# Kernel tuning notes

Hardware: AMD Instinct MI355X
Metric: run time of the kernel (lower is better)

The kernel has to match this reference:

```python
import jax, jax.numpy as jnp
import numpy as np

B, T, H, N_CLASSES = 2048, 128, 64, 32
N_STEPS = 10  # euler micro-steps over t in [0,1], step_size=0.1


def setup_inputs() -> dict:
    key = jax.random.key(0)
    ks = jax.random.split(key, 16)
    s = lambda fan_in: 1.0 / np.sqrt(fan_in)
    inp = {
        "times": jax.random.uniform(ks[0], (B, T), jnp.float32),
        "marks": jax.random.randint(ks[1], (B, T, 1), 0, N_CLASSES),
        "mask": jnp.ones((B, T), jnp.float32),
        # Diffeq.net: MLP(H+1 -> H -> H -> H), Tanh activations, Tanh final
        "W0": jax.random.uniform(ks[2], (H, H + 1), jnp.float32, -s(H + 1), s(H + 1)),
        "b0": jax.random.uniform(ks[3], (H,), jnp.float32, -s(H + 1), s(H + 1)),
        "W1": jax.random.uniform(ks[4], (H, H), jnp.float32, -s(H), s(H)),
        "b1": jax.random.uniform(ks[5], (H,), jnp.float32, -s(H), s(H)),
        "W2": jax.random.uniform(ks[6], (H, H), jnp.float32, -s(H), s(H)),
        "b2": jax.random.uniform(ks[7], (H,), jnp.float32, -s(H), s(H)),
        # Diffeq.intensity: Linear(H -> 1) + Softplus
        "Wi": jax.random.uniform(ks[8], (1, H), jnp.float32, -s(H), s(H)),
        "bi": jax.random.uniform(ks[9], (1,), jnp.float32, -s(H), s(H)) + 0.5,
        # Embedding(n_classes, H)
        "emb": jax.random.normal(ks[10], (N_CLASSES, H), jnp.float32),
        # LSTMCell(1+H, H)
        "W_ih": jax.random.uniform(ks[11], (4 * H, 1 + H), jnp.float32, -s(H), s(H)),
        "W_hh": jax.random.uniform(ks[12], (4 * H, H), jnp.float32, -s(H), s(H)),
        "b_ih": jax.random.uniform(ks[13], (4 * H,), jnp.float32, -s(H), s(H)),
        "b_hh": jax.random.uniform(ks[14], (4 * H,), jnp.float32, -s(H), s(H)),
    }
    return inp


def reference(times, marks, mask, W0, b0, W1, b1, W2, b2, Wi, bi, emb,
              W_ih, W_hh, b_ih, b_hh):
    dt = jnp.float32(1.0 / N_STEPS)

    def mlp(x):  # Diffeq.net
        x = jnp.tanh(x @ W0.T + b0)
        x = jnp.tanh(x @ W1.T + b1)
        return jnp.tanh(x @ W2.T + b2)

    def intensity(h):  # Diffeq.intensity (Softplus head) -> (B,1)
        return jax.nn.softplus(h @ Wi.T + bi)

    # faithful to original: marks[:, 1] is used at every timestep
    m1 = emb[marks[:, 1, 0]]  # (B,H)

    def step(carry, t_col):
        h, c = carry                       # (B,H), (B,H)
        t = t_col[:, None]                 # (B,1) -- diff (event time)
        # fixed-step euler solve of the Diffeq over s in [0,1]
        def euler(state, s):
            hh, integ = state
            s_t = (s * dt) * t             # (B,1) integration time scaled
            d_h = mlp(jnp.concatenate([s_t, hh], -1)) * t
            d_i = intensity(hh) * t
            return (hh + dt * d_h, integ + dt * d_i), None
        (h_ode, integ), _ = jax.lax.scan(
            euler, (h, jnp.zeros_like(t)),
            jnp.arange(N_STEPS, dtype=times.dtype))
        inten = intensity(h_ode)           # (B,1)
        # LSTMCell update with input [t, mark_embedding]
        x_in = jnp.concatenate([t, m1], -1)           # (B,1+H)
        gates = x_in @ W_ih.T + b_ih + h_ode @ W_hh.T + b_hh
        i_g, f_g, g_g, o_g = jnp.split(gates, 4, -1)
        c_new = jax.nn.sigmoid(f_g) * c + jax.nn.sigmoid(i_g) * jnp.tanh(g_g)
        h_new = jax.nn.sigmoid(o_g) * jnp.tanh(c_new)
        nll = (-jnp.log(inten) + integ)[:, 0]          # (B,)
        return (h_new, c_new), (h_ode, nll)

    h0 = jnp.zeros((times.shape[0], emb.shape[1]), times.dtype)
    _, (hidden, nll) = jax.lax.scan(step, (h0, h0), times.T)
    hidden = jnp.transpose(hidden, (1, 0, 2))   # (B,T,H)
    nll = nll.T                                  # (B,T)
    loss = (nll * mask).sum() / mask.sum()
    return loss, hidden
```

## Files before the change

kernel.cpp:

```cpp
#include <hip/hip_runtime.h>


#define T_LEN 128

typedef float  f32x4  __attribute__((ext_vector_type(4)));
typedef __bf16 bf16x8 __attribute__((ext_vector_type(8)));
typedef __bf16 bf16x2 __attribute__((ext_vector_type(2)));

#define MFMA16(a, b, c) __builtin_amdgcn_mfma_f32_16x16x32_bf16((a), (b), (c), 0, 0, 0)

__device__ __forceinline__ float rcp_f(float x) { return __builtin_amdgcn_rcpf(x); }
__device__ __forceinline__ float exp2_f(float x) { return __builtin_amdgcn_exp2f(x); }
__device__ __forceinline__ float log2_f(float x) { return __builtin_amdgcn_logf(x); }

constexpr float kL2E = 1.44269504088896340736f;
constexpr float kLN2 = 0.69314718055994530942f;

__device__ __forceinline__ float tanh_fast(float x) {
  float e = exp2_f(x * (2.0f * kL2E));
  return 1.0f - 2.0f * rcp_f(e + 1.0f);
}
__device__ __forceinline__ float sigm_fast(float x) {
  return rcp_f(1.0f + exp2_f(-kL2E * x));
}
__device__ __forceinline__ float softplus_fast(float x) {
  float neg = log2_f(1.0f + exp2_f(-kL2E * fabsf(x))) * kLN2;
  return fmaxf(x, 0.0f) + neg;
}
__device__ __forceinline__ unsigned packbf(float a, float b) {
  bf16x2 v; v[0] = (__bf16)a; v[1] = (__bf16)b;
  return __builtin_bit_cast(unsigned, v);
}

__launch_bounds__(256)
__global__ void jumpode_main(
    const float* __restrict__ times, const int* __restrict__ marks,
    const float* __restrict__ maskp, const float* __restrict__ W0,
    const float* __restrict__ b0,    const float* __restrict__ W1,
    const float* __restrict__ b1,    const float* __restrict__ W2,
    const float* __restrict__ b2,    const float* __restrict__ Wi,
    const float* __restrict__ bi,    const float* __restrict__ emb,
    const float* __restrict__ W_ih,  const float* __restrict__ W_hh,
    const float* __restrict__ b_ih,  const float* __restrict__ b_hh,
    float* __restrict__ out, float* __restrict__ ws)
{
  __shared__ __align__(16) unsigned whh_l[256 * 32];
  __shared__ __align__(16) float    gm1_l[8 * 256];
  __shared__ __align__(16) unsigned xb0[16 * 32];
  __shared__ __align__(16) unsigned xb1[16 * 32];
  __shared__ __align__(16) unsigned xb2[16 * 32];
  __shared__ __align__(16) float    pint[3][16 * 4];
  __shared__ __align__(16) float    b0_l[64], b1_l[64], b2_l[64];
  __shared__ __align__(16) float    w0c0_l[64];
  __shared__ __align__(16) float    wihc0_l[256];
  __shared__ __align__(16) float    emb16[8][64];
  __shared__ __align__(16) float    tim_l[8][T_LEN];
  __shared__ __align__(16) float    msk_l[8][T_LEN];

  const int tid = threadIdx.x;
  const int wv  = tid >> 6;
  const int l   = tid & 63;
  const int b   = l & 15;
  const int q   = l >> 4;
  const int bm  = b & 7;
  const int row = blockIdx.x * 8 + bm;
  const int xsw = b & 7;

  if (tid < 64) {
    b0_l[tid] = b0[tid]; b1_l[tid] = b1[tid]; b2_l[tid] = b2[tid];
    w0c0_l[tid] = W0[tid * 65];
  }
  wihc0_l[tid] = W_ih[tid * 65];
  for (int idx = tid; idx < 512; idx += 256) {
    int rr = idx >> 6, cc = idx & 63;
    int mk = marks[(blockIdx.x * 8 + rr) * T_LEN + 1];
    emb16[rr][cc] = emb[mk * 64 + cc];
  }
  for (int idx = tid; idx < 1024; idx += 256) {
    int rr = idx >> 7, cc = idx & 127;
    tim_l[rr][cc] = times[(blockIdx.x * 8 + rr) * T_LEN + cc];
    msk_l[rr][cc] = maskp[(blockIdx.x * 8 + rr) * T_LEN + cc];
  }
  #pragma unroll 4
  for (int i = 0; i < 32; ++i) {
    int idx = i * 256 + tid;
    int rw = idx >> 5, c2 = idx & 31;
    unsigned pw = packbf(W_hh[rw * 64 + 2 * c2], W_hh[rw * 64 + 2 * c2 + 1]);
    int gr = c2 >> 2;
    whh_l[rw * 32 + ((gr ^ (rw & 7)) << 2) + (c2 & 3)] = pw;
  }
  __syncthreads();

  {
    int g = tid;
    float acc[8];
    #pragma unroll
    for (int bb = 0; bb < 8; ++bb) acc[bb] = 0.0f;
    const float* wr = &W_ih[g * 65 + 1];
    for (int k = 0; k < 64; ++k) {
      float w = wr[k];
      #pragma unroll
      for (int bb = 0; bb < 8; ++bb) acc[bb] += w * emb16[bb][k];
    }
    float bias = b_ih[g] + b_hh[g];
    int gg = g >> 2;
    #pragma unroll
    for (int bb = 0; bb < 8; ++bb)
      gm1_l[bb * 256 + ((gg ^ bb) << 2) + (g & 3)] = acc[bb] + bias;
  }

  bf16x8 w0f[2], w1f[2], w2f[2];
  {
    const int fm = 16 * wv + b;
    #pragma unroll
    for (int kt = 0; kt < 2; ++kt) {
      const float* r0 = &W0[fm * 65 + 1 + kt * 32 + q * 8];
      const float* r1 = &W1[fm * 64 +     kt * 32 + q * 8];
      const float* r2 = &W2[fm * 64 +     kt * 32 + q * 8];
      bf16x8 a, bb, c;
      #pragma unroll
      for (int e = 0; e < 8; ++e) {
        a[e] = (__bf16)r0[e]; bb[e] = (__bf16)r1[e]; c[e] = (__bf16)r2[e];
      }
      w0f[kt] = a; w1f[kt] = bb; w2f[kt] = c;
    }
  }
  f32x4 wiv;
  #pragma unroll
  for (int r = 0; r < 4; ++r) wiv[r] = Wi[16 * wv + 4 * q + r];
  const float bi_s = bi[0];
  const f32x4 b0v = *(const f32x4*)&b0_l[16 * wv + 4 * q];
  const f32x4 b1v = *(const f32x4*)&b1_l[16 * wv + 4 * q];
  const f32x4 b2v = *(const f32x4*)&b2_l[16 * wv + 4 * q];
  const f32x4 c0v = *(const f32x4*)&w0c0_l[16 * wv + 4 * q];
  const f32x4 zf  = (f32x4){0.f, 0.f, 0.f, 0.f};
  __syncthreads();

  auto write_x = [&](unsigned* buf, const f32x4 v) {
    int gr = (2 * wv + (q >> 1)) ^ xsw;
    int wb = b * 32 + (gr << 2) + ((q & 1) << 1);
    buf[wb]     = packbf(v[0], v[1]);
    buf[wb + 1] = packbf(v[2], v[3]);
  };
  auto read_bfrag = [&](const unsigned* buf, int kt) -> bf16x8 {
    int gr = (kt * 4 + q) ^ xsw;
    return *(const bf16x8*)((const char*)buf + b * 128 + gr * 16);
  };
  auto whh_frag = [&](int R, int kt) -> bf16x8 {
    int rw = R * 16 + b;
    int gr = (kt * 4 + q) ^ xsw;
    return *(const bf16x8*)((const char*)whh_l + rw * 128 + gr * 16);
  };
  auto ld_gm1 = [&](int R) -> f32x4 {
    int gr = (R * 4 + q) ^ bm;
    return *(const f32x4*)((const char*)gm1_l + bm * 1024 + gr * 16);
  };
  auto isect_partial = [&](float* pb, const f32x4 v) {
    float part = wiv[0] * v[0] + wiv[1] * v[1] + wiv[2] * v[2] + wiv[3] * v[3];
    part += __shfl_xor(part, 16);
    part += __shfl_xor(part, 32);
    if (l < 16) pb[b * 4 + wv] = part;
  };

  f32x4 hst = zf, cst = zf;
  float nll_acc = 0.f, m_acc = 0.f;
  const float sel0 = (q == 0 && b < 8) ? 1.0f : 0.0f;

  f32x4 hh;
  float integ, dtt, st, tb;

  auto euler_substep = [&](unsigned* BA, unsigned* BB, float* PB) {
    isect_partial(PB, hh);
    write_x(BA, hh);
    __syncthreads();
    bf16x8 Bf0 = read_bfrag(BA, 0), Bf1 = read_bfrag(BA, 1);

    f32x4 cin;
    #pragma unroll
    for (int r = 0; r < 4; ++r) cin[r] = b0v[r] + c0v[r] * st;
    f32x4 a0 = MFMA16(w0f[0], Bf0, cin);
    f32x4 a1 = MFMA16(w0f[1], Bf1, zf);
    if (wv == 0) {
      f32x4 p = *(const f32x4*)&PB[b * 4];
      integ += dtt * softplus_fast(p[0] + p[1] + p[2] + p[3] + bi_s);
    }
    f32x4 y;
    #pragma unroll
    for (int r = 0; r < 4; ++r) y[r] = tanh_fast(a0[r] + a1[r]);
    write_x(BB, y);
    __syncthreads();
    Bf0 = read_bfrag(BB, 0); Bf1 = read_bfrag(BB, 1);

    a0 = MFMA16(w1f[0], Bf0, b1v);
    a1 = MFMA16(w1f[1], Bf1, zf);
    #pragma unroll
    for (int r = 0; r < 4; ++r) y[r] = tanh_fast(a0[r] + a1[r]);
    write_x(BA, y);
    __syncthreads();
    Bf0 = read_bfrag(BA, 0); Bf1 = read_bfrag(BA, 1);

    a0 = MFMA16(w2f[0], Bf0, b2v);
    a1 = MFMA16(w2f[1], Bf1, zf);
    #pragma unroll
    for (int r = 0; r < 4; ++r) hh[r] += dtt * tanh_fast(a0[r] + a1[r]);
    st += dtt;
  };

  #pragma unroll 1
  for (int step = 0; step < T_LEN; ++step) {
    tb  = tim_l[bm][step];
    dtt = 0.1f * tb;
    hh  = hst;
    integ = 0.f;
    st  = 0.f;

    #pragma unroll 1
    for (int s2 = 0; s2 < 5; ++s2) {
      euler_substep(xb0, xb1, pint[0]);
      euler_substep(xb1, xb0, pint[1]);
    }

    isect_partial(pint[2], hh);
    write_x(xb2, hh);
    if (b < 8) {
      size_t obase = 1 + (((size_t)row) * T_LEN + step) * 64 + 16 * wv + 4 * q;
      out[obase + 0] = hh[0]; out[obase + 1] = hh[1];
      out[obase + 2] = hh[2]; out[obase + 3] = hh[3];
    }
    __syncthreads();
    bf16x8 Bf0 = read_bfrag(xb2, 0), Bf1 = read_bfrag(xb2, 1);

    f32x4 ga[4];
    #pragma unroll
    for (int g = 0; g < 4; ++g) {
      const int Rb = 4 * g + wv;
      f32x4 gm = ld_gm1(Rb);
      f32x4 wc = *(const f32x4*)&wihc0_l[Rb * 16 + q * 4];
      f32x4 cin;
      #pragma unroll
      for (int r = 0; r < 4; ++r) cin[r] = gm[r] + wc[r] * tb;
      f32x4 a = MFMA16(whh_frag(Rb, 0), Bf0, cin);
      ga[g] = MFMA16(whh_frag(Rb, 1), Bf1, a);
    }
    if (wv == 0) {
      f32x4 p = *(const f32x4*)&pint[2][b * 4];
      float inten = softplus_fast(p[0] + p[1] + p[2] + p[3] + bi_s);
      float nll = -(log2_f(inten) * kLN2) + integ;
      float mval = msk_l[bm][step];
      nll_acc += sel0 * mval * nll;
      m_acc   += sel0 * mval;
    }
    #pragma unroll
    for (int r = 0; r < 4; ++r) {
      float ig = sigm_fast(ga[0][r]), fg = sigm_fast(ga[1][r]);
      float gg = tanh_fast(ga[2][r]), og = sigm_fast(ga[3][r]);
      float cn = fg * cst[r] + ig * gg;
      cst[r] = cn;
      hst[r] = og * tanh_fast(cn);
    }
  }

  if (wv == 0) {
    #pragma unroll
    for (int off = 1; off < 64; off <<= 1) {
      nll_acc += __shfl_xor(nll_acc, off);
      m_acc   += __shfl_xor(m_acc, off);
    }
    if (tid == 0) {
      atomicAdd(&ws[0], nll_acc);
      atomicAdd(&ws[1], m_acc);
    }
  }
}

__global__ void jumpode_fin(const float* __restrict__ ws, float* __restrict__ out) {
  if (threadIdx.x == 0 && blockIdx.x == 0) out[0] = ws[0] / ws[1];
}

extern "C" void kernel_launch(void* const* d_in, const int* in_sizes, int n_in,
                              void* d_out, int out_size, void* d_ws, size_t ws_size,
                              hipStream_t stream) {
  (void)in_sizes; (void)n_in; (void)out_size; (void)ws_size;
  const float* times = (const float*)d_in[0];
  const int*   marks = (const int*)  d_in[1];
  const float* maskp = (const float*)d_in[2];
  const float* W0    = (const float*)d_in[3];
  const float* b0    = (const float*)d_in[4];
  const float* W1    = (const float*)d_in[5];
  const float* b1    = (const float*)d_in[6];
  const float* W2    = (const float*)d_in[7];
  const float* b2    = (const float*)d_in[8];
  const float* Wi    = (const float*)d_in[9];
  const float* bi    = (const float*)d_in[10];
  const float* emb   = (const float*)d_in[11];
  const float* W_ih  = (const float*)d_in[12];
  const float* W_hh  = (const float*)d_in[13];
  const float* b_ih  = (const float*)d_in[14];
  const float* b_hh  = (const float*)d_in[15];
  float* out = (float*)d_out;
  float* ws  = (float*)d_ws;

  (void)hipMemsetAsync(d_ws, 0, 2 * sizeof(float), stream);
  jumpode_main<<<dim3(256), dim3(256), 0, stream>>>(
      times, marks, maskp, W0, b0, W1, b1, W2, b2, Wi, bi, emb,
      W_ih, W_hh, b_ih, b_hh, out, ws);
  jumpode_fin<<<dim3(1), dim3(64), 0, stream>>>(ws, out);
}
```

Measured before the change: 1.006 ms.

## Use two waves per block with four batch rows, 512 blocks

Splits work so each block handles 4 batch rows with 2 waves (128 threads), each wave computing two 16-row output tiles of every MLP and gate matmul. The launch goes from 256 to 512 blocks, so all CUs on the device get work and each block synchronises fewer waves per barrier. In exchange each wave does twice the MFMA and activation work per substep, holds more registers, and the MFMA columns are now only a quarter occupied by real rows instead of half.

```diff
diff --git a/kernel.cpp b/kernel.cpp
--- a/kernel.cpp
+++ b/kernel.cpp
@@ -32,7 +32,7 @@
   return __builtin_bit_cast(unsigned, v);
 }
 
-__launch_bounds__(256)
+__launch_bounds__(128)
 __global__ void jumpode_main(
     const float* __restrict__ times, const int* __restrict__ marks,
     const float* __restrict__ maskp, const float* __restrict__ W0,
@@ -45,45 +45,45 @@
     float* __restrict__ out, float* __restrict__ ws)
 {
   __shared__ __align__(16) unsigned whh_l[256 * 32];
-  __shared__ __align__(16) float    gm1_l[8 * 256];
+  __shared__ __align__(16) float    gm1_l[4 * 256];
   __shared__ __align__(16) unsigned xb0[16 * 32];
   __shared__ __align__(16) unsigned xb1[16 * 32];
   __shared__ __align__(16) unsigned xb2[16 * 32];
-  __shared__ __align__(16) float    pint[3][16 * 4];
+  __shared__ __align__(16) float    pint[3][16 * 2];
   __shared__ __align__(16) float    b0_l[64], b1_l[64], b2_l[64];
   __shared__ __align__(16) float    w0c0_l[64];
   __shared__ __align__(16) float    wihc0_l[256];
-  __shared__ __align__(16) float    emb16[8][64];
-  __shared__ __align__(16) float    tim_l[8][T_LEN];
-  __shared__ __align__(16) float    msk_l[8][T_LEN];
+  __shared__ __align__(16) float    emb16[4][64];
+  __shared__ __align__(16) float    tim_l[4][T_LEN];
+  __shared__ __align__(16) float    msk_l[4][T_LEN];
 
   const int tid = threadIdx.x;
   const int wv  = tid >> 6;
   const int l   = tid & 63;
   const int b   = l & 15;
   const int q   = l >> 4;
-  const int bm  = b & 7;
-  const int row = blockIdx.x * 8 + bm;
+  const int bm  = b & 3;
+  const int row = blockIdx.x * 4 + bm;
   const int xsw = b & 7;
 
   if (tid < 64) {
     b0_l[tid] = b0[tid]; b1_l[tid] = b1[tid]; b2_l[tid] = b2[tid];
     w0c0_l[tid] = W0[tid * 65];
   }
-  wihc0_l[tid] = W_ih[tid * 65];
-  for (int idx = tid; idx < 512; idx += 256) {
+  for (int idx = tid; idx < 256; idx += 128) wihc0_l[idx] = W_ih[idx * 65];
+  for (int idx = tid; idx < 256; idx += 128) {
     int rr = idx >> 6, cc = idx & 63;
-    int mk = marks[(blockIdx.x * 8 + rr) * T_LEN + 1];
+    int mk = marks[(blockIdx.x * 4 + rr) * T_LEN + 1];
     emb16[rr][cc] = emb[mk * 64 + cc];
   }
-  for (int idx = tid; idx < 1024; idx += 256) {
+  for (int idx = tid; idx < 512; idx += 128) {
     int rr = idx >> 7, cc = idx & 127;
-    tim_l[rr][cc] = times[(blockIdx.x * 8 + rr) * T_LEN + cc];
-    msk_l[rr][cc] = maskp[(blockIdx.x * 8 + rr) * T_LEN + cc];
+    tim_l[rr][cc] = times[(blockIdx.x * 4 + rr) * T_LEN + cc];
+    msk_l[rr][cc] = maskp[(blockIdx.x * 4 + rr) * T_LEN + cc];
   }
   #pragma unroll 4
-  for (int i = 0; i < 32; ++i) {
-    int idx = i * 256 + tid;
+  for (int i = 0; i < 64; ++i) {
+    int idx = i * 128 + tid;
     int rw = idx >> 5, c2 = idx & 31;
     unsigned pw = packbf(W_hh[rw * 64 + 2 * c2], W_hh[rw * 64 + 2 * c2 + 1]);
     int gr = c2 >> 2;
@@ -91,27 +91,27 @@
   }
   __syncthreads();
 
-  {
-    int g = tid;
-    float acc[8];
-    #pragma unroll
-    for (int bb = 0; bb < 8; ++bb) acc[bb] = 0.0f;
+  for (int g = tid; g < 256; g += 128) {
+    float acc[4];
+    #pragma unroll
+    for (int bb = 0; bb < 4; ++bb) acc[bb] = 0.0f;
     const float* wr = &W_ih[g * 65 + 1];
     for (int k = 0; k < 64; ++k) {
       float w = wr[k];
       #pragma unroll
-      for (int bb = 0; bb < 8; ++bb) acc[bb] += w * emb16[bb][k];
+      for (int bb = 0; bb < 4; ++bb) acc[bb] += w * emb16[bb][k];
     }
     float bias = b_ih[g] + b_hh[g];
     int gg = g >> 2;
     #pragma unroll
-    for (int bb = 0; bb < 8; ++bb)
+    for (int bb = 0; bb < 4; ++bb)
       gm1_l[bb * 256 + ((gg ^ bb) << 2) + (g & 3)] = acc[bb] + bias;
   }
 
-  bf16x8 w0f[2], w1f[2], w2f[2];
-  {
-    const int fm = 16 * wv + b;
+  bf16x8 w0f[2][2], w1f[2][2], w2f[2][2];
+  #pragma unroll
+  for (int j = 0; j < 2; ++j) {
+    const int fm = 16 * (2 * wv + j) + b;
     #pragma unroll
     for (int kt = 0; kt < 2; ++kt) {
       const float* r0 = &W0[fm * 65 + 1 + kt * 32 + q * 8];
@@ -122,25 +122,32 @@
       for (int e = 0; e < 8; ++e) {
         a[e] = (__bf16)r0[e]; bb[e] = (__bf16)r1[e]; c[e] = (__bf16)r2[e];
       }
-      w0f[kt] = a; w1f[kt] = bb; w2f[kt] = c;
-    }
-  }
-  f32x4 wiv;
+      w0f[j][kt] = a; w1f[j][kt] = bb; w2f[j][kt] = c;
+    }
+  }
+  f32x4 wiv[2], b0v[2], b1v[2], b2v[2], c0v[2];
   #pragma unroll
-  for (int r = 0; r < 4; ++r) wiv[r] = Wi[16 * wv + 4 * q + r];
+  for (int j = 0; j < 2; ++j) {
+    const int fb = 16 * (2 * wv + j) + 4 * q;
+    #pragma unroll
+    for (int r = 0; r < 4; ++r) wiv[j][r] = Wi[fb + r];
+    b0v[j] = *(const f32x4*)&b0_l[fb];
+    b1v[j] = *(const f32x4*)&b1_l[fb];
+    b2v[j] = *(const f32x4*)&b2_l[fb];
+    c0v[j] = *(const f32x4*)&w0c0_l[fb];
+  }
   const float bi_s = bi[0];
-  const f32x4 b0v = *(const f32x4*)&b0_l[16 * wv + 4 * q];
-  const f32x4 b1v = *(const f32x4*)&b1_l[16 * wv + 4 * q];
-  const f32x4 b2v = *(const f32x4*)&b2_l[16 * wv + 4 * q];
-  const f32x4 c0v = *(const f32x4*)&w0c0_l[16 * wv + 4 * q];
-  const f32x4 zf  = (f32x4){0.f, 0.f, 0.f, 0.f};
+  const f32x4 zf = (f32x4){0.f, 0.f, 0.f, 0.f};
   __syncthreads();
 
-  auto write_x = [&](unsigned* buf, const f32x4 v) {
-    int gr = (2 * wv + (q >> 1)) ^ xsw;
-    int wb = b * 32 + (gr << 2) + ((q & 1) << 1);
-    buf[wb]     = packbf(v[0], v[1]);
-    buf[wb + 1] = packbf(v[2], v[3]);
+  auto write_x = [&](unsigned* buf, const f32x4* v) {
+    #pragma unroll
+    for (int j = 0; j < 2; ++j) {
+      int gr = (2 * (2 * wv + j) + (q >> 1)) ^ xsw;
+      int wb = b * 32 + (gr << 2) + ((q & 1) << 1);
+      buf[wb]     = packbf(v[j][0], v[j][1]);
+      buf[wb + 1] = packbf(v[j][2], v[j][3]);
+    }
   };
   auto read_bfrag = [&](const unsigned* buf, int kt) -> bf16x8 {
     int gr = (kt * 4 + q) ^ xsw;
@@ -155,18 +162,22 @@
     int gr = (R * 4 + q) ^ bm;
     return *(const f32x4*)((const char*)gm1_l + bm * 1024 + gr * 16);
   };
-  auto isect_partial = [&](float* pb, const f32x4 v) {
-    float part = wiv[0] * v[0] + wiv[1] * v[1] + wiv[2] * v[2] + wiv[3] * v[3];
+  auto isect_partial = [&](float* pb, const f32x4* v) {
+    float part = 0.f;
+    #pragma unroll
+    for (int j = 0; j < 2; ++j)
+      #pragma unroll
+      for (int r = 0; r < 4; ++r) part += wiv[j][r] * v[j][r];
     part += __shfl_xor(part, 16);
     part += __shfl_xor(part, 32);
-    if (l < 16) pb[b * 4 + wv] = part;
-  };
-
-  f32x4 hst = zf, cst = zf;
+    if (l < 16) pb[b * 2 + wv] = part;
+  };
+
+  f32x4 hst[2] = {zf, zf}, cst[2] = {zf, zf};
   float nll_acc = 0.f, m_acc = 0.f;
-  const float sel0 = (q == 0 && b < 8) ? 1.0f : 0.0f;
-
-  f32x4 hh;
+  const float sel0 = (wv == 0 && q == 0 && b < 4) ? 1.0f : 0.0f;
+
+  f32x4 hh[2];
   float integ, dtt, st, tb;
 
   auto euler_substep = [&](unsigned* BA, unsigned* BB, float* PB) {
@@ -175,34 +186,49 @@
     __syncthreads();
     bf16x8 Bf0 = read_bfrag(BA, 0), Bf1 = read_bfrag(BA, 1);
 
-    f32x4 cin;
-    #pragma unroll
-    for (int r = 0; r < 4; ++r) cin[r] = b0v[r] + c0v[r] * st;
-    f32x4 a0 = MFMA16(w0f[0], Bf0, cin);
-    f32x4 a1 = MFMA16(w0f[1], Bf1, zf);
-    if (wv == 0) {
-      f32x4 p = *(const f32x4*)&PB[b * 4];
-      integ += dtt * softplus_fast(p[0] + p[1] + p[2] + p[3] + bi_s);
-    }
-    f32x4 y;
-    #pragma unroll
-    for (int r = 0; r < 4; ++r) y[r] = tanh_fast(a0[r] + a1[r]);
+    f32x4 a0[2], a1[2];
+    #pragma unroll
+    for (int j = 0; j < 2; ++j) {
+      f32x4 cin;
+      #pragma unroll
+      for (int r = 0; r < 4; ++r) cin[r] = b0v[j][r] + c0v[j][r] * st;
+      a0[j] = MFMA16(w0f[j][0], Bf0, cin);
+      a1[j] = MFMA16(w0f[j][1], Bf1, zf);
+    }
+    {
+      integ += dtt * softplus_fast(PB[b * 2] + PB[b * 2 + 1] + bi_s);
+    }
+    f32x4 y[2];
+    #pragma unroll
+    for (int j = 0; j < 2; ++j)
+      #pragma unroll
+      for (int r = 0; r < 4; ++r) y[j][r] = tanh_fast(a0[j][r] + a1[j][r]);
     write_x(BB, y);
     __syncthreads();
     Bf0 = read_bfrag(BB, 0); Bf1 = read_bfrag(BB, 1);
 
-    a0 = MFMA16(w1f[0], Bf0, b1v);
-    a1 = MFMA16(w1f[1], Bf1, zf);
-    #pragma unroll
-    for (int r = 0; r < 4; ++r) y[r] = tanh_fast(a0[r] + a1[r]);
+    #pragma unroll
+    for (int j = 0; j < 2; ++j) {
+      a0[j] = MFMA16(w1f[j][0], Bf0, b1v[j]);
+      a1[j] = MFMA16(w1f[j][1], Bf1, zf);
+    }
+    #pragma unroll
+    for (int j = 0; j < 2; ++j)
+      #pragma unroll
+      for (int r = 0; r < 4; ++r) y[j][r] = tanh_fast(a0[j][r] + a1[j][r]);
     write_x(BA, y);
     __syncthreads();
     Bf0 = read_bfrag(BA, 0); Bf1 = read_bfrag(BA, 1);
 
-    a0 = MFMA16(w2f[0], Bf0, b2v);
-    a1 = MFMA16(w2f[1], Bf1, zf);
-    #pragma unroll
-    for (int r = 0; r < 4; ++r) hh[r] += dtt * tanh_fast(a0[r] + a1[r]);
+    #pragma unroll
+    for (int j = 0; j < 2; ++j) {
+      a0[j] = MFMA16(w2f[j][0], Bf0, b2v[j]);
+      a1[j] = MFMA16(w2f[j][1], Bf1, zf);
+    }
+    #pragma unroll
+    for (int j = 0; j < 2; ++j)
+      #pragma unroll
+      for (int r = 0; r < 4; ++r) hh[j][r] += dtt * tanh_fast(a0[j][r] + a1[j][r]);
     st += dtt;
   };
 
@@ -210,7 +236,7 @@
   for (int step = 0; step < T_LEN; ++step) {
     tb  = tim_l[bm][step];
     dtt = 0.1f * tb;
-    hh  = hst;
+    hh[0] = hst[0]; hh[1] = hst[1];
     integ = 0.f;
     st  = 0.f;
 
@@ -222,42 +248,50 @@
 
     isect_partial(pint[2], hh);
     write_x(xb2, hh);
-    if (b < 8) {
-      size_t obase = 1 + (((size_t)row) * T_LEN + step) * 64 + 16 * wv + 4 * q;
-      out[obase + 0] = hh[0]; out[obase + 1] = hh[1];
-      out[obase + 2] = hh[2]; out[obase + 3] = hh[3];
+    if (b < 4) {
+      size_t obase = 1 + (((size_t)row) * T_LEN + step) * 64 + 4 * q;
+      #pragma unroll
+      for (int j = 0; j < 2; ++j) {
+        size_t o = obase + 16 * (2 * wv + j);
+        out[o + 0] = hh[j][0]; out[o + 1] = hh[j][1];
+        out[o + 2] = hh[j][2]; out[o + 3] = hh[j][3];
+      }
     }
     __syncthreads();
     bf16x8 Bf0 = read_bfrag(xb2, 0), Bf1 = read_bfrag(xb2, 1);
 
-    f32x4 ga[4];
+    f32x4 ga[4][2];
     #pragma unroll
     for (int g = 0; g < 4; ++g) {
-      const int Rb = 4 * g + wv;
-      f32x4 gm = ld_gm1(Rb);
-      f32x4 wc = *(const f32x4*)&wihc0_l[Rb * 16 + q * 4];
-      f32x4 cin;
-      #pragma unroll
-      for (int r = 0; r < 4; ++r) cin[r] = gm[r] + wc[r] * tb;
-      f32x4 a = MFMA16(whh_frag(Rb, 0), Bf0, cin);
-      ga[g] = MFMA16(whh_frag(Rb, 1), Bf1, a);
-    }
-    if (wv == 0) {
-      f32x4 p = *(const f32x4*)&pint[2][b * 4];
-      float inten = softplus_fast(p[0] + p[1] + p[2] + p[3] + bi_s);
+      #pragma unroll
+      for (int j = 0; j < 2; ++j) {
+        const int Rb = 4 * g + 2 * wv + j;
+        f32x4 gm = ld_gm1(Rb);
+        f32x4 wc = *(const f32x4*)&wihc0_l[Rb * 16 + q * 4];
+        f32x4 cin;
+        #pragma unroll
+        for (int r = 0; r < 4; ++r) cin[r] = gm[r] + wc[r] * tb;
+        f32x4 a = MFMA16(whh_frag(Rb, 0), Bf0, cin);
+        ga[g][j] = MFMA16(whh_frag(Rb, 1), Bf1, a);
+      }
+    }
+    {
+      float inten = softplus_fast(pint[2][b * 2] + pint[2][b * 2 + 1] + bi_s);
       float nll = -(log2_f(inten) * kLN2) + integ;
       float mval = msk_l[bm][step];
       nll_acc += sel0 * mval * nll;
       m_acc   += sel0 * mval;
     }
     #pragma unroll
-    for (int r = 0; r < 4; ++r) {
-      float ig = sigm_fast(ga[0][r]), fg = sigm_fast(ga[1][r]);
-      float gg = tanh_fast(ga[2][r]), og = sigm_fast(ga[3][r]);
-      float cn = fg * cst[r] + ig * gg;
-      cst[r] = cn;
-      hst[r] = og * tanh_fast(cn);
-    }
+    for (int j = 0; j < 2; ++j)
+      #pragma unroll
+      for (int r = 0; r < 4; ++r) {
+        float ig = sigm_fast(ga[0][j][r]), fg = sigm_fast(ga[1][j][r]);
+        float gg = tanh_fast(ga[2][j][r]), og = sigm_fast(ga[3][j][r]);
+        float cn = fg * cst[j][r] + ig * gg;
+        cst[j][r] = cn;
+        hst[j][r] = og * tanh_fast(cn);
+      }
   }
 
   if (wv == 0) {
@@ -301,7 +335,7 @@
   float* ws  = (float*)d_ws;
 
   (void)hipMemsetAsync(d_ws, 0, 2 * sizeof(float), stream);
-  jumpode_main<<<dim3(256), dim3(256), 0, stream>>>(
+  jumpode_main<<<dim3(512), dim3(128), 0, stream>>>(
       times, marks, maskp, W0, b0, W1, b1, W2, b2, Wi, bi, emb,
       W_ih, W_hh, b_ih, b_hh, out, ws);
   jumpode_fin<<<dim3(1), dim3(64), 0, stream>>>(ws, out);
```

Result: slower. 1.361 ms (+35.3%).

## Compute first MLP layer redundantly per wave to cut block barriers per Euler substep

Applied to the files above, without the earlier changes.

Each wave now computes all 64 outputs of the first MLP layer, using all four W0 row tiles held in registers. It passes the result through a per-wave private LDS buffer with only an lgkmcnt wait, so that layer needs no block-wide __syncthreads. This brings the barriers per Euler substep down from three to two. The LSTM-step handoff is restructured so the state buffer and intensity partials are published once per step. The cost is four times the layer-0 MFMA and tanh work per wave, plus extra registers for the replicated weights and biases.

```diff
diff --git a/kernel.cpp b/kernel.cpp
--- a/kernel.cpp
+++ b/kernel.cpp
@@ -9,6 +9,9 @@
 
 #define MFMA16(a, b, c) __builtin_amdgcn_mfma_f32_16x16x32_bf16((a), (b), (c), 0, 0, 0)
 
+__device__ __forceinline__ void lds_fence() {
+  asm volatile("s_waitcnt lgkmcnt(0)" ::: "memory");
+}
 __device__ __forceinline__ float rcp_f(float x) { return __builtin_amdgcn_rcpf(x); }
 __device__ __forceinline__ float exp2_f(float x) { return __builtin_amdgcn_exp2f(x); }
 __device__ __forceinline__ float log2_f(float x) { return __builtin_amdgcn_logf(x); }
@@ -46,9 +49,10 @@
 {
   __shared__ __align__(16) unsigned whh_l[256 * 32];
   __shared__ __align__(16) float    gm1_l[8 * 256];
-  __shared__ __align__(16) unsigned xb0[16 * 32];
-  __shared__ __align__(16) unsigned xb1[16 * 32];
-  __shared__ __align__(16) unsigned xb2[16 * 32];
+  __shared__ __align__(16) unsigned bufA[16 * 32];
+  __shared__ __align__(16) unsigned bufB[16 * 32];
+  __shared__ __align__(16) unsigned bufC[16 * 32];
+  __shared__ __align__(16) unsigned xpriv[4 * 16 * 32];
   __shared__ __align__(16) float    pint[3][16 * 4];
   __shared__ __align__(16) float    b0_l[64], b1_l[64], b2_l[64];
   __shared__ __align__(16) float    w0c0_l[64];
@@ -109,42 +113,69 @@
       gm1_l[bb * 256 + ((gg ^ bb) << 2) + (g & 3)] = acc[bb] + bias;
   }
 
-  bf16x8 w0f[2], w1f[2], w2f[2];
+  bf16x8 w0f[4][2];
+  #pragma unroll
+  for (int jt = 0; jt < 4; ++jt) {
+    const int fm = 16 * jt + b;
+    #pragma unroll
+    for (int kt = 0; kt < 2; ++kt) {
+      const float* r0 = &W0[fm * 65 + 1 + kt * 32 + q * 8];
+      bf16x8 a;
+      #pragma unroll
+      for (int e = 0; e < 8; ++e) a[e] = (__bf16)r0[e];
+      w0f[jt][kt] = a;
+    }
+  }
+  bf16x8 w1f[2], w2f[2];
   {
     const int fm = 16 * wv + b;
     #pragma unroll
     for (int kt = 0; kt < 2; ++kt) {
-      const float* r0 = &W0[fm * 65 + 1 + kt * 32 + q * 8];
-      const float* r1 = &W1[fm * 64 +     kt * 32 + q * 8];
-      const float* r2 = &W2[fm * 64 +     kt * 32 + q * 8];
-      bf16x8 a, bb, c;
-      #pragma unroll
-      for (int e = 0; e < 8; ++e) {
-        a[e] = (__bf16)r0[e]; bb[e] = (__bf16)r1[e]; c[e] = (__bf16)r2[e];
-      }
-      w0f[kt] = a; w1f[kt] = bb; w2f[kt] = c;
-    }
+      const float* r1 = &W1[fm * 64 + kt * 32 + q * 8];
+      const float* r2 = &W2[fm * 64 + kt * 32 + q * 8];
+      bf16x8 bb, c;
+      #pragma unroll
+      for (int e = 0; e < 8; ++e) { bb[e] = (__bf16)r1[e]; c[e] = (__bf16)r2[e]; }
+      w1f[kt] = bb; w2f[kt] = c;
+    }
+  }
+  f32x4 b0a[4], c0a[4];
+  #pragma unroll
+  for (int jt = 0; jt < 4; ++jt) {
+    b0a[jt] = *(const f32x4*)&b0_l[16 * jt + 4 * q];
+    c0a[jt] = *(const f32x4*)&w0c0_l[16 * jt + 4 * q];
   }
   f32x4 wiv;
   #pragma unroll
   for (int r = 0; r < 4; ++r) wiv[r] = Wi[16 * wv + 4 * q + r];
   const float bi_s = bi[0];
-  const f32x4 b0v = *(const f32x4*)&b0_l[16 * wv + 4 * q];
   const f32x4 b1v = *(const f32x4*)&b1_l[16 * wv + 4 * q];
   const f32x4 b2v = *(const f32x4*)&b2_l[16 * wv + 4 * q];
-  const f32x4 c0v = *(const f32x4*)&w0c0_l[16 * wv + 4 * q];
   const f32x4 zf  = (f32x4){0.f, 0.f, 0.f, 0.f};
-  __syncthreads();
-
-  auto write_x = [&](unsigned* buf, const f32x4 v) {
+
+  auto write_pub = [&](unsigned* buf, const f32x4 v) {
     int gr = (2 * wv + (q >> 1)) ^ xsw;
     int wb = b * 32 + (gr << 2) + ((q & 1) << 1);
     buf[wb]     = packbf(v[0], v[1]);
     buf[wb + 1] = packbf(v[2], v[3]);
   };
-  auto read_bfrag = [&](const unsigned* buf, int kt) -> bf16x8 {
+  auto read_frag = [&](const unsigned* buf, int kt) -> bf16x8 {
     int gr = (kt * 4 + q) ^ xsw;
     return *(const bf16x8*)((const char*)buf + b * 128 + gr * 16);
+  };
+  auto write_priv = [&](const f32x4* v) {
+    unsigned* base = &xpriv[wv * 512];
+    #pragma unroll
+    for (int jt = 0; jt < 4; ++jt) {
+      int gr = (2 * jt + (q >> 1)) ^ xsw;
+      int wb = b * 32 + (gr << 2) + ((q & 1) << 1);
+      base[wb]     = packbf(v[jt][0], v[jt][1]);
+      base[wb + 1] = packbf(v[jt][2], v[jt][3]);
+    }
+  };
+  auto read_priv = [&](int kt) -> bf16x8 {
+    int gr = (kt * 4 + q) ^ xsw;
+    return *(const bf16x8*)((const char*)&xpriv[wv * 512] + b * 128 + gr * 16);
   };
   auto whh_frag = [&](int R, int kt) -> bf16x8 {
     int rw = R * 16 + b;
@@ -155,81 +186,83 @@
     int gr = (R * 4 + q) ^ bm;
     return *(const f32x4*)((const char*)gm1_l + bm * 1024 + gr * 16);
   };
-  auto isect_partial = [&](float* pb, const f32x4 v) {
+  auto isect_pub = [&](float* pb, const f32x4 v) {
     float part = wiv[0] * v[0] + wiv[1] * v[1] + wiv[2] * v[2] + wiv[3] * v[3];
     part += __shfl_xor(part, 16);
     part += __shfl_xor(part, 32);
     if (l < 16) pb[b * 4 + wv] = part;
   };
 
-  f32x4 hst = zf, cst = zf;
-  float nll_acc = 0.f, m_acc = 0.f;
+  f32x4 hso = zf, cso = zf;
+  f32x4 hho = zf;
+  float nll_acc = 0.f, m_acc = 0.f, integ = 0.f, dtt = 0.f, tb = 0.f;
   const float sel0 = (q == 0 && b < 8) ? 1.0f : 0.0f;
 
-  f32x4 hh;
-  float integ, dtt, st, tb;
-
-  auto euler_substep = [&](unsigned* BA, unsigned* BB, float* PB) {
-    isect_partial(PB, hh);
-    write_x(BA, hh);
+  write_pub(bufC, zf);
+  if (l < 16) pint[2][b * 4 + wv] = 0.f;
+  __syncthreads();
+
+  auto phaseA = [&](const unsigned* HB, const float* PB, int sub) {
+    bf16x8 H0 = read_frag(HB, 0), H1 = read_frag(HB, 1);
+    const float stv = (float)sub * dtt;
+    f32x4 y1[4];
+    #pragma unroll
+    for (int jt = 0; jt < 4; ++jt) {
+      f32x4 cin;
+      #pragma unroll
+      for (int r = 0; r < 4; ++r) cin[r] = b0a[jt][r] + c0a[jt][r] * stv;
+      f32x4 a = MFMA16(w0f[jt][0], H0, cin);
+      a = MFMA16(w0f[jt][1], H1, a);
+      #pragma unroll
+      for (int r = 0; r < 4; ++r) y1[jt][r] = tanh_fast(a[r]);
+    }
+    if (wv == 0) {
+      integ += dtt * softplus_fast(PB[b * 4] + PB[b * 4 + 1] +
+                                   PB[b * 4 + 2] + PB[b * 4 + 3] + bi_s);
+    }
+    write_priv(y1);
+    lds_fence();
+    bf16x8 Y0 = read_priv(0), Y1 = read_priv(1);
+    f32x4 a = MFMA16(w1f[0], Y0, b1v);
+    a = MFMA16(w1f[1], Y1, a);
+    f32x4 y2;
+    #pragma unroll
+    for (int r = 0; r < 4; ++r) y2[r] = tanh_fast(a[r]);
+    write_pub(bufA, y2);
     __syncthreads();
-    bf16x8 Bf0 = read_bfrag(BA, 0), Bf1 = read_bfrag(BA, 1);
-
-    f32x4 cin;
-    #pragma unroll
-    for (int r = 0; r < 4; ++r) cin[r] = b0v[r] + c0v[r] * st;
-    f32x4 a0 = MFMA16(w0f[0], Bf0, cin);
-    f32x4 a1 = MFMA16(w0f[1], Bf1, zf);
-    if (wv == 0) {
-      f32x4 p = *(const f32x4*)&PB[b * 4];
-      integ += dtt * softplus_fast(p[0] + p[1] + p[2] + p[3] + bi_s);
-    }
-    f32x4 y;
-    #pragma unroll
-    for (int r = 0; r < 4; ++r) y[r] = tanh_fast(a0[r] + a1[r]);
-    write_x(BB, y);
+  };
+  auto phaseB = [&](float* PP) {
+    bf16x8 Y0 = read_frag(bufA, 0), Y1 = read_frag(bufA, 1);
+    f32x4 a = MFMA16(w2f[0], Y0, b2v);
+    a = MFMA16(w2f[1], Y1, a);
+    #pragma unroll
+    for (int r = 0; r < 4; ++r) hho[r] += dtt * tanh_fast(a[r]);
+    isect_pub(PP, hho);
+    write_pub(bufB, hho);
     __syncthreads();
-    Bf0 = read_bfrag(BB, 0); Bf1 = read_bfrag(BB, 1);
-
-    a0 = MFMA16(w1f[0], Bf0, b1v);
-    a1 = MFMA16(w1f[1], Bf1, zf);
-    #pragma unroll
-    for (int r = 0; r < 4; ++r) y[r] = tanh_fast(a0[r] + a1[r]);
-    write_x(BA, y);
-    __syncthreads();
-    Bf0 = read_bfrag(BA, 0); Bf1 = read_bfrag(BA, 1);
-
-    a0 = MFMA16(w2f[0], Bf0, b2v);
-    a1 = MFMA16(w2f[1], Bf1, zf);
-    #pragma unroll
-    for (int r = 0; r < 4; ++r) hh[r] += dtt * tanh_fast(a0[r] + a1[r]);
-    st += dtt;
   };
 
   #pragma unroll 1
   for (int step = 0; step < T_LEN; ++step) {
     tb  = tim_l[bm][step];
     dtt = 0.1f * tb;
-    hh  = hst;
+    hho = hso;
     integ = 0.f;
-    st  = 0.f;
-
-    #pragma unroll 1
-    for (int s2 = 0; s2 < 5; ++s2) {
-      euler_substep(xb0, xb1, pint[0]);
-      euler_substep(xb1, xb0, pint[1]);
-    }
-
-    isect_partial(pint[2], hh);
-    write_x(xb2, hh);
+
+    phaseA(bufC, pint[2], 0); phaseB(pint[0]);
+    #pragma unroll
+    for (int sp = 0; sp < 4; ++sp) {
+      phaseA(bufB, pint[0], 2 * sp + 1); phaseB(pint[1]);
+      phaseA(bufB, pint[1], 2 * sp + 2); phaseB(pint[0]);
+    }
+    phaseA(bufB, pint[0], 9); phaseB(pint[1]);
+
+    bf16x8 H0 = read_frag(bufB, 0), H1 = read_frag(bufB, 1);
     if (b < 8) {
       size_t obase = 1 + (((size_t)row) * T_LEN + step) * 64 + 16 * wv + 4 * q;
-      out[obase + 0] = hh[0]; out[obase + 1] = hh[1];
-      out[obase + 2] = hh[2]; out[obase + 3] = hh[3];
-    }
-    __syncthreads();
-    bf16x8 Bf0 = read_bfrag(xb2, 0), Bf1 = read_bfrag(xb2, 1);
-
+      out[obase + 0] = hho[0]; out[obase + 1] = hho[1];
+      out[obase + 2] = hho[2]; out[obase + 3] = hho[3];
+    }
     f32x4 ga[4];
     #pragma unroll
     for (int g = 0; g < 4; ++g) {
@@ -239,12 +272,12 @@
       f32x4 cin;
       #pragma unroll
       for (int r = 0; r < 4; ++r) cin[r] = gm[r] + wc[r] * tb;
-      f32x4 a = MFMA16(whh_frag(Rb, 0), Bf0, cin);
-      ga[g] = MFMA16(whh_frag(Rb, 1), Bf1, a);
+      f32x4 a = MFMA16(whh_frag(Rb, 0), H0, cin);
+      ga[g] = MFMA16(whh_frag(Rb, 1), H1, a);
     }
     if (wv == 0) {
-      f32x4 p = *(const f32x4*)&pint[2][b * 4];
-      float inten = softplus_fast(p[0] + p[1] + p[2] + p[3] + bi_s);
+      const float* pp = &pint[1][b * 4];
+      float inten = softplus_fast(pp[0] + pp[1] + pp[2] + pp[3] + bi_s);
       float nll = -(log2_f(inten) * kLN2) + integ;
       float mval = msk_l[bm][step];
       nll_acc += sel0 * mval * nll;
@@ -254,10 +287,13 @@
     for (int r = 0; r < 4; ++r) {
       float ig = sigm_fast(ga[0][r]), fg = sigm_fast(ga[1][r]);
       float gg = tanh_fast(ga[2][r]), og = sigm_fast(ga[3][r]);
-      float cn = fg * cst[r] + ig * gg;
-      cst[r] = cn;
-      hst[r] = og * tanh_fast(cn);
-    }
+      float cn = fg * cso[r] + ig * gg;
+      cso[r] = cn;
+      hso[r] = og * tanh_fast(cn);
+    }
+    write_pub(bufC, hso);
+    isect_pub(pint[2], hso);
+    __syncthreads();
   }
 
   if (wv == 0) {
```

Result: slower. 1.335 ms (+32.8%).
